# Kernel optimization log

Hardware: AMD Instinct MI355X
Metric: run time of the kernel (lower is better)

Reference implementation:

```python
import jax, jax.numpy as jnp
import numpy as np

BS, L, H, D = 4, 1024, 12, 768   # docs, seq len, attn heads, hidden
NE, M, P = 42, 96, 42 * 42        # max entities (min_height), mentions/doc, ht pairs
OFFSET = 1                        # bert/roberta [CLS] offset


def setup_inputs() -> dict:
    key = jax.random.key(0)
    k1, k2, k3, k4, k5 = jax.random.split(key, 5)
    sequence_output = jax.random.normal(k1, (BS, L, D), jnp.float32)
    attention = jax.random.uniform(k2, (BS, H, L, L), jnp.float32)
    mention_pos = jax.random.randint(k3, (BS, M), 0, L - OFFSET - 1).astype(jnp.int32)
    mention_entity = jnp.sort(jax.random.randint(k4, (BS, M), 0, NE), axis=-1).astype(jnp.int32)
    hts = jax.random.randint(k5, (BS, P, 2), 0, NE).astype(jnp.int32)
    return {"sequence_output": sequence_output, "attention": attention,
            "mention_pos": mention_pos, "mention_entity": mention_entity, "hts": hts}


def _per_doc_entities(seq, att, pos, ent):
    # seq [L,D], att [H,L,L], pos [M] mention token idx, ent [M] entity segment id
    idx = pos + OFFSET
    m_emb = seq[idx]                              # [M,D]  gathered mention embeddings
    m_att = jnp.transpose(att[:, idx], (1, 0, 2))  # [M,H,L] gathered mention attentions
    counts = jax.ops.segment_sum(jnp.ones((M,), seq.dtype), ent, num_segments=NE)
    has = counts > 0
    # mean-pool attentions per entity (zeros for empty entities, as in torch code)
    e_att = jax.ops.segment_sum(m_att, ent, num_segments=NE) / jnp.maximum(counts, 1.0)[:, None, None]
    # stable logsumexp-pool embeddings per entity
    seg_max = jax.ops.segment_max(m_emb, ent, num_segments=NE)      # -inf for empty segments
    seg_max = jnp.where(has[:, None], seg_max, 0.0)
    seg_sum = jax.ops.segment_sum(jnp.exp(m_emb - seg_max[ent]), ent, num_segments=NE)
    e_emb = jnp.where(has[:, None], jnp.log(jnp.maximum(seg_sum, 1e-30)) + seg_max, 0.0)
    return e_emb, e_att                           # [NE,D], [NE,H,L]


def _channel_map(seq, e_att):
    # all-pairs (h_att * t_att).mean(heads), normalize over tokens, contract with seq
    pair = jnp.einsum('ahl,bhl->abl', e_att, e_att) / H      # [NE,NE,L]
    pair = pair / (pair.sum(-1, keepdims=True) + 1e-5)
    return jnp.einsum('abl,ld->abd', pair, seq)              # [NE,NE,D]


def reference(sequence_output, attention, mention_pos, mention_entity, hts):
    e_emb, e_att = jax.vmap(_per_doc_entities)(sequence_output, attention,
                                               mention_pos, mention_entity)
    hss = jax.vmap(lambda emb, ht: emb[ht[:, 0]])(e_emb, hts).reshape(BS * P, D)
    tss = jax.vmap(lambda emb, ht: emb[ht[:, 1]])(e_emb, hts).reshape(BS * P, D)
    feature_map = jax.vmap(_channel_map)(sequence_output, e_att)  # [BS,NE,NE,D]
    return hss, tss, feature_map
```

## Files before the change

### kernel.cpp

```cpp
#include <hip/hip_runtime.h>
#include <hip/hip_bf16.h>

#define BSZ   4
#define LSEQ  1024
#define NH    12
#define DDIM  768
#define NEN   42
#define NM    96
#define NPAIR (NEN*NEN)
#define OFF   1

typedef short bf16x8 __attribute__((ext_vector_type(8)));
typedef float f32x4  __attribute__((ext_vector_type(4)));

__device__ __forceinline__ float bf2f(unsigned short u) {
    union { unsigned u; float f; } c; c.u = ((unsigned)u) << 16; return c.f;
}
__device__ __forceinline__ unsigned char f2fp8(float v) {
    int r = __builtin_amdgcn_cvt_pk_fp8_f32(v, 0.f, 0, false);
    return (unsigned char)(r & 0xFF);
}

typedef const __attribute__((address_space(1))) unsigned int glb_u32;
typedef __attribute__((address_space(3))) unsigned int lds_u32;
__device__ __forceinline__ void glds16(const void* g, void* l) {
    __builtin_amdgcn_global_load_lds((glb_u32*)g, (lds_u32*)l, 16, 0, 0);
}

#define NLC   4
#define EMB_CNT  (BSZ*NEN*DDIM)
#define PSUM_CNT (BSZ*NLC*NPAIR)
#define EATT_CNT (BSZ*NEN*NH*LSEQ)
#define PTIL_BYTES ((size_t)BSZ*NPAIR*LSEQ)

#define ATT_TOTAL (BSZ*NEN*NH)

#define TEN   6
#define NTILE 7
#define NTRIT (NTILE*(NTILE+1)/2)
#define LCHK  256
#define PAIR_BLKS (NTRIT*NLC*BSZ)
#define T_BLKS    ((LSEQ/32)*(DDIM/32)*BSZ)
#define EMB_BLKS  (BSZ*NEN*3)
#define MID2_TOTAL (PAIR_BLKS + T_BLKS + EMB_BLKS)

#define BM 128
#define BN 64
#define BK 64
#define MT 14
#define NT (DDIM/BN)
#define FMAP_BLKS (MT*NT*BSZ)
#define GATH_BLKS (BSZ*NPAIR/4)
#define TAIL_TOTAL (FMAP_BLKS + GATH_BLKS)

__global__ __launch_bounds__(256) void att_kernel(
        const float* __restrict__ att,
        const int* __restrict__ mpos,
        const int* __restrict__ ment,
        __hip_bfloat16* __restrict__ e_att) {
    __shared__ int sp[NM];
    __shared__ int se[NM];
    int id = blockIdx.x;
    int h = id % NH;
    int e = (id / NH) % NEN;
    int b = id / (NH * NEN);
    int t = threadIdx.x;
    if (t < NM) { sp[t] = mpos[b*NM + t] + OFF; se[t] = ment[b*NM + t]; }
    __syncthreads();
    const float* ab = att + ((size_t)(b*NH + h)) * LSEQ * LSEQ;
    float4 acc = {0.f, 0.f, 0.f, 0.f};
    int cnt = 0;
    for (int m = 0; m < NM; ++m) {
        if (se[m] == e) {
            ++cnt;
            float4 v = ((const float4*)(ab + (size_t)sp[m]*LSEQ))[t];
            acc.x += v.x; acc.y += v.y; acc.z += v.z; acc.w += v.w;
        }
    }
    float inv = cnt ? 1.f / (float)cnt : 0.f;
    union { ushort4 u4; __hip_bfloat16 hh[4]; } pk;
    pk.hh[0] = __float2bfloat16(acc.x * inv);
    pk.hh[1] = __float2bfloat16(acc.y * inv);
    pk.hh[2] = __float2bfloat16(acc.z * inv);
    pk.hh[3] = __float2bfloat16(acc.w * inv);
    ((ushort4*)(e_att + ((size_t)(b*NEN + e)*NH + h)*LSEQ))[t] = pk.u4;
}

__global__ __launch_bounds__(256) void mid2_kernel(
        const float* __restrict__ seq,
        const __hip_bfloat16* __restrict__ e_att,
        const int* __restrict__ mpos,
        const int* __restrict__ ment,
        unsigned char* __restrict__ ptil,
        float* __restrict__ psum,
        unsigned char* __restrict__ seqT,
        float* __restrict__ e_emb) {
    __shared__ __align__(16) char smraw[4352];
    const int bid = blockIdx.x;
    const int t = threadIdx.x;

    if (bid < PAIR_BLKS) {
        int tri = bid % NTRIT;
        int lc  = (bid / NTRIT) % NLC;
        int b   = bid / (NTRIT * NLC);
        int ta = 0, rem = tri;
        while (rem >= NTILE - ta) { rem -= NTILE - ta; ++ta; }
        int tb = ta + rem;
        int l = lc * LCHK + t;

        const __hip_bfloat16* ebase = e_att + (size_t)b*NEN*NH*LSEQ + l;
        float s[TEN][TEN];
        #pragma unroll
        for (int i = 0; i < TEN; ++i)
            #pragma unroll
            for (int j = 0; j < TEN; ++j) s[i][j] = 0.f;

        #pragma unroll 4
        for (int h = 0; h < NH; ++h) {
            float xa[TEN], xb[TEN];
            #pragma unroll
            for (int e = 0; e < TEN; ++e)
                xa[e] = bf2f(*(const unsigned short*)(ebase + ((size_t)(ta*TEN+e)*NH + h)*LSEQ));
            #pragma unroll
            for (int e = 0; e < TEN; ++e)
                xb[e] = bf2f(*(const unsigned short*)(ebase + ((size_t)(tb*TEN+e)*NH + h)*LSEQ));
            #pragma unroll
            for (int i = 0; i < TEN; ++i)
                #pragma unroll
                for (int j = 0; j < TEN; ++j)
                    s[i][j] += xa[i] * xb[j];
        }

        unsigned char* pbase = ptil + (size_t)b*NPAIR*LSEQ + l;
        #pragma unroll
        for (int i = 0; i < TEN; ++i) {
            #pragma unroll
            for (int j = 0; j < TEN; ++j) {
                unsigned char q = f2fp8(s[i][j]);
                int pa = ta*TEN + i, pb = tb*TEN + j;
                pbase[(size_t)(pa*NEN + pb)*LSEQ] = q;
                if (ta != tb)
                    pbase[(size_t)(pb*NEN + pa)*LSEQ] = q;
            }
        }

        int lane = t & 63, w = t >> 6;
        float (*redp)[TEN*TEN] = (float(*)[TEN*TEN])smraw;
        float keep = 0.f;
        #pragma unroll
        for (int i = 0; i < TEN; ++i) {
            #pragma unroll
            for (int j = 0; j < TEN; ++j) {
                float v = s[i][j];
                v += __shfl_xor(v,  1, 64);
                v += __shfl_xor(v,  2, 64);
                v += __shfl_xor(v,  4, 64);
                v += __shfl_xor(v,  8, 64);
                v += __shfl_xor(v, 16, 64);
                v += __shfl_xor(v, 32, 64);
                if (lane == i*TEN + j) keep = v;
            }
        }
        if (lane < TEN*TEN) redp[w][lane] = keep;
        __syncthreads();
        if (t < TEN*TEN) {
            float v = redp[0][t] + redp[1][t] + redp[2][t] + redp[3][t];
            int i = t / TEN, j = t % TEN;
            int pa = ta*TEN + i, pb = tb*TEN + j;
            float* ps = psum + ((size_t)(b*NLC + lc))*NPAIR;
            ps[pa*NEN + pb] = v;
            if (ta != tb) ps[pb*NEN + pa] = v;
        }
    } else if (bid < PAIR_BLKS + T_BLKS) {
        int id = bid - PAIR_BLKS;
        int l0 = (id % (LSEQ/32)) * 32;
        int d0 = ((id / (LSEQ/32)) % (DDIM/32)) * 32;
        int b  = id / ((LSEQ/32) * (DDIM/32));
        float (*tile)[33] = (float(*)[33])smraw;
        int l = t >> 3, dq = (t & 7) * 4;
        float4 v = *(const float4*)(seq + ((size_t)b*LSEQ + l0 + l)*DDIM + d0 + dq);
        tile[l][dq+0] = v.x; tile[l][dq+1] = v.y;
        tile[l][dq+2] = v.z; tile[l][dq+3] = v.w;
        __syncthreads();
        int d = t >> 3, lq = (t & 7) * 4;
        int w = __builtin_amdgcn_cvt_pk_fp8_f32(tile[lq+0][d], tile[lq+1][d], 0, false);
        w     = __builtin_amdgcn_cvt_pk_fp8_f32(tile[lq+2][d], tile[lq+3][d], w, true);
        *(int*)(seqT + ((size_t)b*DDIM + d0 + d)*LSEQ + l0 + lq) = w;
    } else {
        int id = bid - PAIR_BLKS - T_BLKS;
        int chunk = id % 3;
        int e = (id / 3) % NEN;
        int b = id / (3 * NEN);
        int* sp   = (int*)smraw;
        int* se   = sp + NM;
        int* list = se + NM;
        int* pcnt = list + NM;
        if (t < NM) { sp[t] = mpos[b*NM + t] + OFF; se[t] = ment[b*NM + t]; }
        __syncthreads();
        if (t == 0) {
            int c = 0;
            for (int m = 0; m < NM; ++m) if (se[m] == e) list[c++] = sp[m];
            pcnt[0] = c;
        }
        __syncthreads();
        int cnt = pcnt[0];
        int d = chunk * 256 + t;
        const float* sq = seq + (size_t)b * LSEQ * DDIM + d;
        float mx = -1e30f;
        for (int m = 0; m < cnt; ++m) mx = fmaxf(mx, sq[(size_t)list[m] * DDIM]);
        float out = 0.f;
        if (cnt) {
            float s = 0.f;
            for (int m = 0; m < cnt; ++m) s += expf(sq[(size_t)list[m] * DDIM] - mx);
            out = logf(fmaxf(s, 1e-30f)) + mx;
        }
        e_emb[((size_t)b*NEN + e)*DDIM + d] = out;
    }
}

__global__ __launch_bounds__(256) void tail_kernel(
        const unsigned char* __restrict__ ptil,
        const unsigned char* __restrict__ seqT,
        const float* __restrict__ psum,
        const float* __restrict__ e_emb,
        const int* __restrict__ hts,
        float* __restrict__ out_h,
        float* __restrict__ out_t,
        float* __restrict__ fmap) {
    __shared__ unsigned char As[2][BM*BK];
    __shared__ unsigned char Bs[2][BN*BK];
    const int bid = blockIdx.x;
    const int t = threadIdx.x;

    if (bid >= FMAP_BLKS) {
        int id4  = bid - FMAP_BLKS;
        int grp  = t >> 6;
        int lane = t & 63;
        int id   = id4 * 4 + grp;
        int b    = id / NPAIR;
        int hi = hts[id*2 + 0];
        int ti = hts[id*2 + 1];
        const float4* eh = (const float4*)(e_emb + ((size_t)(b*NEN + hi))*DDIM);
        const float4* et = (const float4*)(e_emb + ((size_t)(b*NEN + ti))*DDIM);
        float4* oh = (float4*)(out_h + (size_t)id*DDIM);
        float4* ot = (float4*)(out_t + (size_t)id*DDIM);
        #pragma unroll
        for (int i = 0; i < 3; ++i) {
            oh[lane + 64*i] = eh[lane + 64*i];
            ot[lane + 64*i] = et[lane + 64*i];
        }
        return;
    }

    int tile = (bid & 7) * (FMAP_BLKS/8) + (bid >> 3);
    const int lane = t & 63;
    const int wid  = t >> 6;
    const int wr   = wid >> 1;
    const int wc   = wid & 1;
    const int bx = tile % MT, by = (tile / MT) % NT, b = tile / (MT*NT);
    const int r0 = bx * BM, c0 = by * BN;

    const unsigned char* Ab  = ptil + (size_t)b * NPAIR * LSEQ;
    const unsigned char* Btb = seqT + (size_t)b * DDIM * LSEQ;
    unsigned char* AsB = (unsigned char*)As;
    unsigned char* BsB = (unsigned char*)Bs;

    const f32x4 zero = {0.f, 0.f, 0.f, 0.f};
    f32x4 acc[4][2];
    #pragma unroll
    for (int m = 0; m < 4; ++m)
        #pragma unroll
        for (int n = 0; n < 2; ++n) acc[m][n] = zero;

    const int fr = lane & 15, kg = lane >> 4;

#define STAGE(buf, k0)                                                        \
    {                                                                         \
        _Pragma("unroll")                                                     \
        for (int i = 0; i < 2; ++i) {                                         \
            int L = t*16 + i*4096;                                            \
            int r = L >> 6, beta = L & 63;                                    \
            glds16(Ab + (size_t)(r0 + r)*LSEQ + (k0)                          \
                      + (beta ^ (((r >> 1) & 3) << 4)),                       \
                   AsB + (buf)*8192 + L);                                     \
        }                                                                     \
        {                                                                     \
            int L = t*16;                                                     \
            int c = L >> 6, beta = L & 63;                                    \
            glds16(Btb + (size_t)(c0 + c)*LSEQ + (k0)                         \
                      + (beta ^ (((c >> 1) & 3) << 4)),                       \
                   BsB + (buf)*4096 + L);                                     \
        }                                                                     \
    }

    STAGE(0, 0);
    __syncthreads();

    int cur = 0;
    for (int ki = 0; ki < LSEQ/BK; ++ki) {
        if (ki + 1 < LSEQ/BK) STAGE(cur ^ 1, (ki + 1) * BK);

        const unsigned char* Ac = AsB + cur*8192;
        const unsigned char* Bc = BsB + cur*4096;

        #pragma unroll
        for (int ks = 0; ks < 2; ++ks) {
            long af[4], bfv[2];
            #pragma unroll
            for (int m = 0; m < 4; ++m) {
                int R = wr*64 + m*16 + fr;
                int e0 = (ks*32 + kg*8) ^ (((R >> 1) & 3) << 4);
                af[m] = *(const long*)(Ac + R*64 + e0);
            }
            #pragma unroll
            for (int n = 0; n < 2; ++n) {
                int C = wc*32 + n*16 + fr;
                int e0 = (ks*32 + kg*8) ^ (((C >> 1) & 3) << 4);
                bfv[n] = *(const long*)(Bc + C*64 + e0);
            }
            #pragma unroll
            for (int m = 0; m < 4; ++m)
                #pragma unroll
                for (int n = 0; n < 2; ++n)
                    acc[m][n] = __builtin_amdgcn_mfma_f32_16x16x32_fp8_fp8(
                                    af[m], bfv[n], acc[m][n], 0, 0, 0);
        }
        __syncthreads();
        cur ^= 1;
    }

    const float* psb = psum + (size_t)b * NLC * NPAIR;
    #pragma unroll
    for (int m = 0; m < 4; ++m) {
        int lr0 = wr*64 + m*16 + kg*4;
        #pragma unroll
        for (int i = 0; i < 4; ++i) {
            int row = r0 + lr0 + i;
            if (row < NPAIR) {
                float S = psb[row] + psb[NPAIR + row]
                        + psb[2*NPAIR + row] + psb[3*NPAIR + row];
                float sc = 1.f / (S + (float)NH * 1e-5f);
                #pragma unroll
                for (int n = 0; n < 2; ++n) {
                    int col = c0 + wc*32 + n*16 + fr;
                    fmap[((size_t)b*NPAIR + row)*DDIM + col] = acc[m][n][i] * sc;
                }
            }
        }
    }
#undef STAGE
}

extern "C" void kernel_launch(void* const* d_in, const int* in_sizes, int n_in,
                              void* d_out, int out_size, void* d_ws, size_t ws_size,
                              hipStream_t stream) {
    const float* seq  = (const float*)d_in[0];
    const float* att  = (const float*)d_in[1];
    const int*   mpos = (const int*)d_in[2];
    const int*   ment = (const int*)d_in[3];
    const int*   hts  = (const int*)d_in[4];

    float* ws_f  = (float*)d_ws;
    float* e_emb = ws_f;
    float* psum  = ws_f + EMB_CNT;
    __hip_bfloat16* e_att = (__hip_bfloat16*)(ws_f + EMB_CNT + PSUM_CNT);
    unsigned char* ptil = (unsigned char*)(e_att + EATT_CNT);
    unsigned char* seqT = ptil + PTIL_BYTES;

    float* out_h = (float*)d_out;
    float* out_t = out_h + (size_t)BSZ*NPAIR*DDIM;
    float* fmap  = out_t + (size_t)BSZ*NPAIR*DDIM;

    hipLaunchKernelGGL(att_kernel, dim3(ATT_TOTAL), dim3(256), 0, stream,
                       att, mpos, ment, e_att);
    hipLaunchKernelGGL(mid2_kernel, dim3(MID2_TOTAL), dim3(256), 0, stream,
                       seq, e_att, mpos, ment, ptil, psum, seqT, e_emb);
    hipLaunchKernelGGL(tail_kernel, dim3(TAIL_TOTAL), dim3(256), 0, stream,
                       ptil, seqT, psum, e_emb, hts, out_h, out_t, fmap);
}
```

Measured before the change: 55.18 us.

## Widen pair-kernel token chunks, double GEMM K-tile, precompact mention lists

Result: faster. 52.49 us (-4.9%).

```diff
diff --git a/kernel.cpp b/kernel.cpp
--- a/kernel.cpp
+++ b/kernel.cpp
@@ -16,10 +16,6 @@
 __device__ __forceinline__ float bf2f(unsigned short u) {
     union { unsigned u; float f; } c; c.u = ((unsigned)u) << 16; return c.f;
 }
-__device__ __forceinline__ unsigned char f2fp8(float v) {
-    int r = __builtin_amdgcn_cvt_pk_fp8_f32(v, 0.f, 0, false);
-    return (unsigned char)(r & 0xFF);
-}
 
 typedef const __attribute__((address_space(1))) unsigned int glb_u32;
 typedef __attribute__((address_space(3))) unsigned int lds_u32;
@@ -27,7 +23,7 @@
     __builtin_amdgcn_global_load_lds((glb_u32*)g, (lds_u32*)l, 16, 0, 0);
 }
 
-#define NLC   4
+#define NLC   2
 #define EMB_CNT  (BSZ*NEN*DDIM)
 #define PSUM_CNT (BSZ*NLC*NPAIR)
 #define EATT_CNT (BSZ*NEN*NH*LSEQ)
@@ -38,7 +34,7 @@
 #define TEN   6
 #define NTILE 7
 #define NTRIT (NTILE*(NTILE+1)/2)
-#define LCHK  256
+#define LCHK  512
 #define PAIR_BLKS (NTRIT*NLC*BSZ)
 #define T_BLKS    ((LSEQ/32)*(DDIM/32)*BSZ)
 #define EMB_BLKS  (BSZ*NEN*3)
@@ -46,7 +42,7 @@
 
 #define BM 128
 #define BN 64
-#define BK 64
+#define BK 128
 #define MT 14
 #define NT (DDIM/BN)
 #define FMAP_BLKS (MT*NT*BSZ)
@@ -60,6 +56,8 @@
         __hip_bfloat16* __restrict__ e_att) {
     __shared__ int sp[NM];
     __shared__ int se[NM];
+    __shared__ int list[NM];
+    __shared__ int pcnt;
     int id = blockIdx.x;
     int h = id % NH;
     int e = (id / NH) % NEN;
@@ -67,15 +65,18 @@
     int t = threadIdx.x;
     if (t < NM) { sp[t] = mpos[b*NM + t] + OFF; se[t] = ment[b*NM + t]; }
     __syncthreads();
+    if (t == 0) {
+        int c = 0;
+        for (int m = 0; m < NM; ++m) if (se[m] == e) list[c++] = sp[m];
+        pcnt = c;
+    }
+    __syncthreads();
+    int cnt = pcnt;
     const float* ab = att + ((size_t)(b*NH + h)) * LSEQ * LSEQ;
     float4 acc = {0.f, 0.f, 0.f, 0.f};
-    int cnt = 0;
-    for (int m = 0; m < NM; ++m) {
-        if (se[m] == e) {
-            ++cnt;
-            float4 v = ((const float4*)(ab + (size_t)sp[m]*LSEQ))[t];
-            acc.x += v.x; acc.y += v.y; acc.z += v.z; acc.w += v.w;
-        }
+    for (int m = 0; m < cnt; ++m) {
+        float4 v = ((const float4*)(ab + (size_t)list[m]*LSEQ))[t];
+        acc.x += v.x; acc.y += v.y; acc.z += v.z; acc.w += v.w;
     }
     float inv = cnt ? 1.f / (float)cnt : 0.f;
     union { ushort4 u4; __hip_bfloat16 hh[4]; } pk;
@@ -106,29 +107,35 @@
         int ta = 0, rem = tri;
         while (rem >= NTILE - ta) { rem -= NTILE - ta; ++ta; }
         int tb = ta + rem;
-        int l = lc * LCHK + t;
+        int l = lc * LCHK + t * 2;
 
         const __hip_bfloat16* ebase = e_att + (size_t)b*NEN*NH*LSEQ + l;
-        float s[TEN][TEN];
+        float sx[TEN][TEN], sy[TEN][TEN];
         #pragma unroll
         for (int i = 0; i < TEN; ++i)
             #pragma unroll
-            for (int j = 0; j < TEN; ++j) s[i][j] = 0.f;
+            for (int j = 0; j < TEN; ++j) { sx[i][j] = 0.f; sy[i][j] = 0.f; }
 
         #pragma unroll 4
         for (int h = 0; h < NH; ++h) {
-            float xa[TEN], xb[TEN];
-            #pragma unroll
-            for (int e = 0; e < TEN; ++e)
-                xa[e] = bf2f(*(const unsigned short*)(ebase + ((size_t)(ta*TEN+e)*NH + h)*LSEQ));
-            #pragma unroll
-            for (int e = 0; e < TEN; ++e)
-                xb[e] = bf2f(*(const unsigned short*)(ebase + ((size_t)(tb*TEN+e)*NH + h)*LSEQ));
+            float xax[TEN], xay[TEN], xbx[TEN], xby[TEN];
+            #pragma unroll
+            for (int e = 0; e < TEN; ++e) {
+                ushort2 u = *(const ushort2*)(ebase + ((size_t)(ta*TEN+e)*NH + h)*LSEQ);
+                xax[e] = bf2f(u.x); xay[e] = bf2f(u.y);
+            }
+            #pragma unroll
+            for (int e = 0; e < TEN; ++e) {
+                ushort2 u = *(const ushort2*)(ebase + ((size_t)(tb*TEN+e)*NH + h)*LSEQ);
+                xbx[e] = bf2f(u.x); xby[e] = bf2f(u.y);
+            }
             #pragma unroll
             for (int i = 0; i < TEN; ++i)
                 #pragma unroll
-                for (int j = 0; j < TEN; ++j)
-                    s[i][j] += xa[i] * xb[j];
+                for (int j = 0; j < TEN; ++j) {
+                    sx[i][j] += xax[i] * xbx[j];
+                    sy[i][j] += xay[i] * xby[j];
+                }
         }
 
         unsigned char* pbase = ptil + (size_t)b*NPAIR*LSEQ + l;
@@ -136,11 +143,12 @@
         for (int i = 0; i < TEN; ++i) {
             #pragma unroll
             for (int j = 0; j < TEN; ++j) {
-                unsigned char q = f2fp8(s[i][j]);
+                int w = __builtin_amdgcn_cvt_pk_fp8_f32(sx[i][j], sy[i][j], 0, false);
+                unsigned short q = (unsigned short)(w & 0xFFFF);
                 int pa = ta*TEN + i, pb = tb*TEN + j;
-                pbase[(size_t)(pa*NEN + pb)*LSEQ] = q;
+                *(unsigned short*)(pbase + (size_t)(pa*NEN + pb)*LSEQ) = q;
                 if (ta != tb)
-                    pbase[(size_t)(pb*NEN + pa)*LSEQ] = q;
+                    *(unsigned short*)(pbase + (size_t)(pb*NEN + pa)*LSEQ) = q;
             }
         }
 
@@ -151,7 +159,7 @@
         for (int i = 0; i < TEN; ++i) {
             #pragma unroll
             for (int j = 0; j < TEN; ++j) {
-                float v = s[i][j];
+                float v = sx[i][j] + sy[i][j];
                 v += __shfl_xor(v,  1, 64);
                 v += __shfl_xor(v,  2, 64);
                 v += __shfl_xor(v,  4, 64);
@@ -277,19 +285,20 @@
 #define STAGE(buf, k0)                                                        \
     {                                                                         \
         _Pragma("unroll")                                                     \
+        for (int i = 0; i < 4; ++i) {                                         \
+            int L = t*16 + i*4096;                                            \
+            int r = L >> 7, beta = L & 127;                                   \
+            glds16(Ab + (size_t)(r0 + r)*LSEQ + (k0)                          \
+                      + (beta ^ ((r & 7) << 4)),                              \
+                   AsB + (buf)*16384 + L);                                    \
+        }                                                                     \
+        _Pragma("unroll")                                                     \
         for (int i = 0; i < 2; ++i) {                                         \
             int L = t*16 + i*4096;                                            \
-            int r = L >> 6, beta = L & 63;                                    \
-            glds16(Ab + (size_t)(r0 + r)*LSEQ + (k0)                          \
-                      + (beta ^ (((r >> 1) & 3) << 4)),                       \
-                   AsB + (buf)*8192 + L);                                     \
-        }                                                                     \
-        {                                                                     \
-            int L = t*16;                                                     \
-            int c = L >> 6, beta = L & 63;                                    \
+            int c = L >> 7, beta = L & 127;                                   \
             glds16(Btb + (size_t)(c0 + c)*LSEQ + (k0)                         \
-                      + (beta ^ (((c >> 1) & 3) << 4)),                       \
-                   BsB + (buf)*4096 + L);                                     \
+                      + (beta ^ ((c & 7) << 4)),                              \
+                   BsB + (buf)*8192 + L);                                     \
         }                                                                     \
     }
 
@@ -300,23 +309,23 @@
     for (int ki = 0; ki < LSEQ/BK; ++ki) {
         if (ki + 1 < LSEQ/BK) STAGE(cur ^ 1, (ki + 1) * BK);
 
-        const unsigned char* Ac = AsB + cur*8192;
-        const unsigned char* Bc = BsB + cur*4096;
-
-        #pragma unroll
-        for (int ks = 0; ks < 2; ++ks) {
+        const unsigned char* Ac = AsB + cur*16384;
+        const unsigned char* Bc = BsB + cur*8192;
+
+        #pragma unroll
+        for (int ks = 0; ks < 4; ++ks) {
             long af[4], bfv[2];
             #pragma unroll
             for (int m = 0; m < 4; ++m) {
                 int R = wr*64 + m*16 + fr;
-                int e0 = (ks*32 + kg*8) ^ (((R >> 1) & 3) << 4);
-                af[m] = *(const long*)(Ac + R*64 + e0);
+                int e0 = (ks*32 + kg*8) ^ ((R & 7) << 4);
+                af[m] = *(const long*)(Ac + R*128 + e0);
             }
             #pragma unroll
             for (int n = 0; n < 2; ++n) {
                 int C = wc*32 + n*16 + fr;
-                int e0 = (ks*32 + kg*8) ^ (((C >> 1) & 3) << 4);
-                bfv[n] = *(const long*)(Bc + C*64 + e0);
+                int e0 = (ks*32 + kg*8) ^ ((C & 7) << 4);
+                bfv[n] = *(const long*)(Bc + C*128 + e0);
             }
             #pragma unroll
             for (int m = 0; m < 4; ++m)
@@ -337,8 +346,7 @@
         for (int i = 0; i < 4; ++i) {
             int row = r0 + lr0 + i;
             if (row < NPAIR) {
-                float S = psb[row] + psb[NPAIR + row]
-                        + psb[2*NPAIR + row] + psb[3*NPAIR + row];
+                float S = psb[row] + psb[NPAIR + row];
                 float sc = 1.f / (S + (float)NH * 1e-5f);
                 #pragma unroll
                 for (int n = 0; n < 2; ++n) {
```
